# Kernel tuning notes

Hardware: AMD Instinct MI355X
Metric: run time of the kernel (lower is better)

The kernel has to match this reference:

```python
import jax, jax.numpy as jnp
import numpy as np

N_HEAD = 16


def setup_inputs() -> dict:
    key = jax.random.key(0)
    k1, k2, k3 = jax.random.split(key, 3)
    B, S, D = 4, 2048, 1024
    scale = 1.0 / np.sqrt(D)
    return {
        "inp": jax.random.normal(k1, (B, S, D), dtype=jnp.float32),
        "w_attn": jax.random.normal(k2, (D, 3 * D), dtype=jnp.float32) * scale,
        "b_attn": jnp.zeros((3 * D,), dtype=jnp.float32),
        "w_proj": jax.random.normal(k3, (D, D), dtype=jnp.float32) * scale,
        "b_proj": jnp.zeros((D,), dtype=jnp.float32),
    }


def reference(inp, w_attn, b_attn, w_proj, b_proj):
    B, S, D = inp.shape
    H = N_HEAD
    hd = D // H
    qkv = inp @ w_attn + b_attn                      # [B,S,3D]
    q, k, v = jnp.split(qkv, 3, axis=-1)
    q = q.reshape(B, S, H, hd)
    k = k.reshape(B, S, H, hd)
    v = v.reshape(B, S, H, hd)
    # scores [B,H,S,S], scaled by 1/sqrt(head_dim)
    scores = jnp.einsum("bqhd,bkhd->bhqk", q, k) / jnp.sqrt(jnp.asarray(hd, dtype=inp.dtype))
    # causal mask: position q attends to k <= q
    causal = jnp.tril(jnp.ones((S, S), dtype=bool))
    scores = jnp.where(causal[None, None], scores, jnp.asarray(-jnp.inf, dtype=scores.dtype))
    probs = jax.nn.softmax(scores, axis=-1)          # dropout omitted (eval mode)
    ctx = jnp.einsum("bhqk,bkhd->bqhd", probs, v).reshape(B, S, D)
    return ctx @ w_proj + b_proj
```

## Files before the change

kernel.cpp:

```cpp
#include <hip/hip_runtime.h>


#define DEV __device__ __forceinline__

typedef unsigned short u16;
typedef unsigned u32x4 __attribute__((ext_vector_type(4)));
typedef u16   u16x8 __attribute__((ext_vector_type(8)));
typedef u16   u16x4 __attribute__((ext_vector_type(4)));
typedef float f32x4v __attribute__((ext_vector_type(4)));
typedef __bf16 bf16x8 __attribute__((ext_vector_type(8)));

#define BB 4
#define SS 2048
#define DD 1024
#define HH 16
#define HD 64
#define MM (BB*SS)
#define N3D (3*DD)
#define C8  0.18033688011112042f

DEV u16 f2bf(float f) { return __builtin_bit_cast(u16, (__bf16)f); }
DEV float bf2f(u16 h) { return __builtin_bit_cast(float, (unsigned)h << 16); }

DEV f32x4v mfma16(u16x8 a, u16x8 b, f32x4v c) {
  return __builtin_amdgcn_mfma_f32_16x16x32_bf16(
      __builtin_bit_cast(bf16x8, a), __builtin_bit_cast(bf16x8, b), c, 0, 0, 0);
}

DEV void async16(const void* g, void* l) {
  __builtin_amdgcn_global_load_lds(
      (const __attribute__((address_space(1))) void*)g,
      (__attribute__((address_space(3))) void*)l, 16, 0, 0);
}

__global__ __launch_bounds__(256) void prep_kernel(
    const float* __restrict__ inp, const float* __restrict__ w_attn,
    const float* __restrict__ w_proj, u16* __restrict__ Abf,
    u16* __restrict__ WAt, u16* __restrict__ WPt) {
  const int bid = blockIdx.x;
  const int tid = threadIdx.x;
  if (bid < 4096) {
    __shared__ float t[32][33];
    const float* W; u16* Wt; int N, K, n0, k0;
    if (bid < 3072) { W = w_attn; Wt = WAt; N = N3D; K = DD;
                      n0 = (bid % 96) * 32; k0 = (bid / 96) * 32; }
    else            { W = w_proj; Wt = WPt; N = DD;  K = DD;
                      int tb = bid - 3072; n0 = (tb % 32) * 32; k0 = (tb / 32) * 32; }
    int tx = tid & 31, ty = tid >> 5;
    for (int i = ty; i < 32; i += 8)
      t[i][tx] = W[(long long)(k0 + i) * N + n0 + tx];
    __syncthreads();
    for (int i = ty; i < 32; i += 8)
      Wt[(long long)(n0 + i) * K + k0 + tx] = f2bf(t[tx][i]);
  } else {
    const long long n = (long long)MM * DD;
    long long i = (long long)(bid - 4096) * 256 + tid;
    for (long long j = i * 4; j < n; j += 2048LL * 256 * 4) {
      f32x4v v = *(const f32x4v*)(inp + j);
      u16x4 o;
      o.x = f2bf(v.x); o.y = f2bf(v.y); o.z = f2bf(v.z); o.w = f2bf(v.w);
      *(u16x4*)(Abf + j) = o;
    }
  }
}

__global__ __launch_bounds__(256) void gemm_kernel(
    const u16* __restrict__ A, const u16* __restrict__ Bt,
    const float* __restrict__ bias, void* __restrict__ Cout,
    u16* __restrict__ Vt, int Ndim, int Kdim, int mode) {
  __shared__ __align__(16) char smem[65536];

  const int tid = threadIdx.x;
  const int lane = tid & 63, wid = tid >> 6;
  const int l15 = lane & 15, lg = lane >> 4;

  const int nwg = (int)(gridDim.x * gridDim.y);
  const int orig = (int)(blockIdx.y * gridDim.x + blockIdx.x);
  const int wg = (orig & 7) * (nwg >> 3) + (orig >> 3);
  const int bx = wg % (int)gridDim.x, by = wg / (int)gridDim.x;
  const int rb = by * 128, cb = bx * 128;
  const int wr = (wid >> 1) * 64, wc = (wid & 1) * 64;

  f32x4v acc[4][4] = {};

  const int rlo = tid >> 3;
  const int cbS = (tid & 7) * 16;
  const int swS = cbS ^ ((rlo & 7) << 4);
  const int sd  = rlo * 128 + cbS;

  const int xr  = (l15 & 7) << 4;
  const int vaA = l15 * 128 + ((lg * 16) ^ xr);
  const int gvA0 = wr * 128 + vaA, gvA1 = gvA0 ^ 64;
  const int gvB0 = wc * 128 + vaA, gvB1 = gvB0 ^ 64;

  const char* pa[4];
  const char* pb[4];
#pragma unroll
  for (int i = 0; i < 4; ++i) {
    pa[i] = (const char*)A  + (long long)(rb + i * 32 + rlo) * (Kdim * 2) + swS;
    pb[i] = (const char*)Bt + (long long)(cb + i * 32 + rlo) * (Kdim * 2) + swS;
  }

  auto stage = [&](int dofs, int kb) {
#pragma unroll
    for (int i = 0; i < 4; ++i) {
      async16(pa[i] + kb, smem + dofs + i * 4096 + sd);
      async16(pb[i] + kb, smem + 32768 + dofs + i * 4096 + sd);
    }
  };

  auto compute = [&](int aofs, int bofs) {
    u16x8 a0[4], b0[4], a1[4], b1[4];
#pragma unroll
    for (int mi = 0; mi < 4; ++mi) {
      a0[mi] = *(const u16x8*)(smem + aofs + mi * 2048 + gvA0);
      a1[mi] = *(const u16x8*)(smem + aofs + mi * 2048 + gvA1);
    }
#pragma unroll
    for (int ni = 0; ni < 4; ++ni) {
      b0[ni] = *(const u16x8*)(smem + bofs + ni * 2048 + gvB0);
      b1[ni] = *(const u16x8*)(smem + bofs + ni * 2048 + gvB1);
    }
#pragma unroll
    for (int mi = 0; mi < 4; ++mi)
#pragma unroll
      for (int ni = 0; ni < 4; ++ni) {
        acc[mi][ni] = mfma16(a0[mi], b0[ni], acc[mi][ni]);
        acc[mi][ni] = mfma16(a1[mi], b1[ni], acc[mi][ni]);
      }
  };

  const int nK = Kdim >> 6;
  stage(0, 0);
  __syncthreads();
  for (int kt = 0; kt < nK; kt += 2) {
    stage(16384, 128);
    compute(0, 32768);
    __syncthreads();
    if (kt + 2 < nK) stage(0, 256);
    compute(16384, 49152);
    __syncthreads();
#pragma unroll
    for (int i = 0; i < 4; ++i) { pa[i] += 256; pb[i] += 256; }
  }

#pragma unroll
  for (int mi = 0; mi < 4; ++mi)
#pragma unroll
    for (int ni = 0; ni < 4; ++ni) {
      int col = cb + wc + ni * 16 + l15;
      float bv = bias[col];
      if (mode == 1 && col >= 2 * DD) {
        int h = (col >> 6) & 15, d = col & 63;
#pragma unroll
        for (int r = 0; r < 4; ++r) {
          int row = rb + wr + mi * 16 + lg * 4 + r;
          int b = row >> 11, s = row & 2047;
          Vt[(((long long)(b * HH + h) * HD + d) << 11) + s] = f2bf(acc[mi][ni][r] + bv);
        }
      } else {
#pragma unroll
        for (int r = 0; r < 4; ++r) {
          int row = rb + wr + mi * 16 + lg * 4 + r;
          float v = acc[mi][ni][r] + bv;
          if (mode) ((u16*)Cout)[(long long)row * Ndim + col] = f2bf(v);
          else      ((float*)Cout)[(long long)row * Ndim + col] = v;
        }
      }
    }
}

__global__ __launch_bounds__(256, 4) void attn_kernel(
    const u16* __restrict__ qkv, const u16* __restrict__ Vt,
    u16* __restrict__ ctx) {
  __shared__ __align__(16) char smem[32768];

  const int tid = threadIdx.x, lane = tid & 63, wid = tid >> 6;
  const int l15 = lane & 15, lg = lane >> 4;

  const int d = (int)blockIdx.x;
  const int rank = d >> 3;
  const int t = rank >> 3;
  const int jj = t & 3, q4 = t >> 2;
  const int qt = (q4 == 0) ? 15 - jj : (q4 == 1) ? 8 + jj
               : (q4 == 2) ? 7 - jj  : jj;
  const int bh = (d & 7) * 8 + (rank & 7);
  const int b = bh >> 4, h = bh & 15;

  const u16* Qcol = qkv + (long long)b * SS * N3D + h * HD;
  const u16* Kcol = qkv + (long long)b * SS * N3D + DD + h * HD;
  const u16* Vbh  = Vt + (long long)bh * HD * SS;

  const int rowA = 8 * (l15 >> 2) + (l15 & 3);
  const int kA = (((l15 & 3) | (((l15 >> 2) & 1) << 2))) << 4;
  const int vk0 = rowA * 128 + ((lg * 16) ^ kA);
  const int vk1 = vk0 ^ 64;
  const int vk2 = vk0 + 512;
  const int vk3 = vk2 ^ 64;
  const int kV = (((l15 & 3) | (((l15 >> 3) & 1) << 2))) << 4;
  const int vv0 = l15 * 128 + ((lg * 16) ^ kV);
  const int vv1 = vv0 ^ 64;

  const int rlo = tid >> 3;
  const int cbS = (tid & 7) * 16;
  const int kw = (((rlo & 3) | (((rlo >> 3) & 1) << 2))) << 4;
  const int swS = cbS ^ kw;
  const int sd  = rlo * 128 + cbS;
  const long long KSTP = 64LL * N3D * 2;
  const long long VSTP = 64LL * 2;
  const long long KHLF = 32LL * N3D * 2;
  const long long VHLF = 32LL * SS * 2;

  auto stage = [&](int dofs, const char* ka, const char* va) {
    async16(ka,        smem + dofs + sd);
    async16(ka + KHLF, smem + dofs + 4096 + sd);
    async16(va,        smem + 16384 + dofs + sd);
    async16(va + VHLF, smem + 16384 + dofs + 4096 + sd);
  };

  const int q0 = qt * 128;
  const int qw = q0 + wid * 32;
  const int nkb = 2 * qt + 2;

  u16x8 qf[2][2];
#pragma unroll
  for (int mi = 0; mi < 2; ++mi)
#pragma unroll
    for (int kk = 0; kk < 2; ++kk)
      qf[mi][kk] = *(const u16x8*)(Qcol + (long long)(qw + mi * 16 + l15) * N3D +
                                   kk * 32 + lg * 8);

  f32x4v acc[2][4] = {};
  float m_s[2] = {-1e30f, -1e30f}, l_p[2] = {0.f, 0.f};

  const char* ka = (const char*)Kcol + (long long)rlo * (N3D * 2) + swS;
  const char* va = (const char*)Vbh + (long long)rlo * (SS * 2) + swS;

  auto compute = [&](int kofs, int vofs, int kbase) {
    if (kbase > qw + 31) return;

    f32x4v pf[2][2][2] = {};
    {
      u16x8 kf0, kf1;
      kf0 = *(const u16x8*)(smem + kofs + vk0);
      kf1 = *(const u16x8*)(smem + kofs + vk1);
      __builtin_amdgcn_s_setprio(1);
      pf[0][0][0] = mfma16(kf0, qf[0][0], pf[0][0][0]);
      pf[0][0][0] = mfma16(kf1, qf[0][1], pf[0][0][0]);
      pf[1][0][0] = mfma16(kf0, qf[1][0], pf[1][0][0]);
      pf[1][0][0] = mfma16(kf1, qf[1][1], pf[1][0][0]);
      __builtin_amdgcn_s_setprio(0);
      kf0 = *(const u16x8*)(smem + kofs + vk2);
      kf1 = *(const u16x8*)(smem + kofs + vk3);
      __builtin_amdgcn_s_setprio(1);
      pf[0][0][1] = mfma16(kf0, qf[0][0], pf[0][0][1]);
      pf[0][0][1] = mfma16(kf1, qf[0][1], pf[0][0][1]);
      pf[1][0][1] = mfma16(kf0, qf[1][0], pf[1][0][1]);
      pf[1][0][1] = mfma16(kf1, qf[1][1], pf[1][0][1]);
      __builtin_amdgcn_s_setprio(0);
      kf0 = *(const u16x8*)(smem + kofs + 4096 + vk0);
      kf1 = *(const u16x8*)(smem + kofs + 4096 + vk1);
      __builtin_amdgcn_s_setprio(1);
      pf[0][1][0] = mfma16(kf0, qf[0][0], pf[0][1][0]);
      pf[0][1][0] = mfma16(kf1, qf[0][1], pf[0][1][0]);
      pf[1][1][0] = mfma16(kf0, qf[1][0], pf[1][1][0]);
      pf[1][1][0] = mfma16(kf1, qf[1][1], pf[1][1][0]);
      __builtin_amdgcn_s_setprio(0);
      kf0 = *(const u16x8*)(smem + kofs + 4096 + vk2);
      kf1 = *(const u16x8*)(smem + kofs + 4096 + vk3);
      __builtin_amdgcn_s_setprio(1);
      pf[0][1][1] = mfma16(kf0, qf[0][0], pf[0][1][1]);
      pf[0][1][1] = mfma16(kf1, qf[0][1], pf[0][1][1]);
      pf[1][1][1] = mfma16(kf0, qf[1][0], pf[1][1][1]);
      pf[1][1][1] = mfma16(kf1, qf[1][1], pf[1][1][1]);
      __builtin_amdgcn_s_setprio(0);
    }

    if (kbase + 63 > qw) {
      const int kl = kbase + lg * 8;
#pragma unroll
      for (int mi = 0; mi < 2; ++mi) {
        const int qg = qw + mi * 16 + l15;
#pragma unroll
        for (int ks = 0; ks < 2; ++ks)
#pragma unroll
          for (int ab = 0; ab < 2; ++ab)
#pragma unroll
            for (int r = 0; r < 4; ++r)
              if (kl + ks * 32 + ab * 4 + r > qg) pf[mi][ks][ab][r] = -1e30f;
      }
    }

    float lmax[2];
    bool need = false;
#pragma unroll
    for (int mi = 0; mi < 2; ++mi) {
      float v0 = fmaxf(fmaxf(fmaxf(pf[mi][0][0][0], pf[mi][0][0][1]),
                             pf[mi][0][0][2]), pf[mi][0][0][3]);
      float v1 = fmaxf(fmaxf(fmaxf(pf[mi][0][1][0], pf[mi][0][1][1]),
                             pf[mi][0][1][2]), pf[mi][0][1][3]);
      float v2 = fmaxf(fmaxf(fmaxf(pf[mi][1][0][0], pf[mi][1][0][1]),
                             pf[mi][1][0][2]), pf[mi][1][0][3]);
      float v3 = fmaxf(fmaxf(fmaxf(pf[mi][1][1][0], pf[mi][1][1][1]),
                             pf[mi][1][1][2]), pf[mi][1][1][3]);
      lmax[mi] = fmaxf(fmaxf(v0, v1), fmaxf(v2, v3));
      need = need || (lmax[mi] > m_s[mi] + 64.f);
    }
    if (__any(need)) {
#pragma unroll
      for (int mi = 0; mi < 2; ++mi) {
        float rm = fmaxf(lmax[mi], __shfl_xor(lmax[mi], 16));
        rm = fmaxf(rm, __shfl_xor(rm, 32));
        float newm = fmaxf(m_s[mi], rm);
        float sc = __builtin_exp2f((m_s[mi] - newm) * C8);
        m_s[mi] = newm;
        l_p[mi] *= sc;
#pragma unroll
        for (int r = 0; r < 4; ++r) {
          float scq = __shfl(sc, (lane & 48) + lg * 4 + r);
#pragma unroll
          for (int di = 0; di < 4; ++di) acc[mi][di][r] *= scq;
        }
      }
    }
#pragma unroll
    for (int mi = 0; mi < 2; ++mi) {
      float mC = m_s[mi] * C8;
      float rsum = 0.f;
#pragma unroll
      for (int ks = 0; ks < 2; ++ks)
#pragma unroll
        for (int ab = 0; ab < 2; ++ab)
#pragma unroll
          for (int r = 0; r < 4; ++r) {
            float p = __builtin_exp2f(__builtin_fmaf(pf[mi][ks][ab][r], C8, -mC));
            pf[mi][ks][ab][r] = p;
            rsum += p;
          }
      l_p[mi] += rsum;
    }

    u16x8 pa[2][2];
#pragma unroll
    for (int mi = 0; mi < 2; ++mi)
#pragma unroll
      for (int ks = 0; ks < 2; ++ks) {
        u32x4 w;
        w.x = (unsigned)f2bf(pf[mi][ks][0][0]) | ((unsigned)f2bf(pf[mi][ks][0][1]) << 16);
        w.y = (unsigned)f2bf(pf[mi][ks][0][2]) | ((unsigned)f2bf(pf[mi][ks][0][3]) << 16);
        w.z = (unsigned)f2bf(pf[mi][ks][1][0]) | ((unsigned)f2bf(pf[mi][ks][1][1]) << 16);
        w.w = (unsigned)f2bf(pf[mi][ks][1][2]) | ((unsigned)f2bf(pf[mi][ks][1][3]) << 16);
        pa[mi][ks] = __builtin_bit_cast(u16x8, w);
      }

#pragma unroll
    for (int di = 0; di < 4; ++di) {
      u16x8 v0 = *(const u16x8*)(smem + vofs + di * 2048 + vv0);
      u16x8 v1 = *(const u16x8*)(smem + vofs + di * 2048 + vv1);
      __builtin_amdgcn_s_setprio(1);
      acc[0][di] = mfma16(pa[0][0], v0, acc[0][di]);
      acc[0][di] = mfma16(pa[0][1], v1, acc[0][di]);
      acc[1][di] = mfma16(pa[1][0], v0, acc[1][di]);
      acc[1][di] = mfma16(pa[1][1], v1, acc[1][di]);
      __builtin_amdgcn_s_setprio(0);
    }
  };

  stage(0, ka, va);
  __syncthreads();

  for (int kb = 0; kb < nkb; kb += 2) {
    stage(8192, ka + KSTP, va + VSTP);
    compute(0, 16384, kb * 64);
    __syncthreads();
    if (kb + 2 < nkb) stage(0, ka + 2 * KSTP, va + 2 * VSTP);
    compute(8192, 24576, (kb + 1) * 64);
    __syncthreads();
    ka += 2 * KSTP; va += 2 * VSTP;
  }

#pragma unroll
  for (int mi = 0; mi < 2; ++mi) {
    float l_red = l_p[mi] + __shfl_xor(l_p[mi], 16);
    l_red += __shfl_xor(l_red, 32);
#pragma unroll
    for (int r = 0; r < 4; ++r) {
      float lq = __shfl(l_red, (lane & 48) + lg * 4 + r);
      float inv = 1.f / lq;
      int qrow = qw + mi * 16 + lg * 4 + r;
#pragma unroll
      for (int di = 0; di < 4; ++di) {
        int dd = di * 16 + l15;
        ctx[((long long)(b * SS + qrow)) * DD + h * HD + dd] = f2bf(acc[mi][di][r] * inv);
      }
    }
  }
}

extern "C" void kernel_launch(void* const* d_in, const int* in_sizes, int n_in,
                              void* d_out, int out_size, void* d_ws, size_t ws_size,
                              hipStream_t stream) {
  const float* inp    = (const float*)d_in[0];
  const float* w_attn = (const float*)d_in[1];
  const float* b_attn = (const float*)d_in[2];
  const float* w_proj = (const float*)d_in[3];
  const float* b_proj = (const float*)d_in[4];
  float* out = (float*)d_out;
  char* ws = (char*)d_ws;

  const long long off_A   = 0;
  const long long off_WAt = 16777216;
  const long long off_WPt = 23068672;
  const long long off_qkv = 25165824;
  const long long off_ctx = 75497472;
  const long long off_Vt  = 92274688;
  const long long need    = 109051904;
  if (ws_size < (size_t)need) return;

  u16* Abf = (u16*)(ws + off_A);
  u16* WAt = (u16*)(ws + off_WAt);
  u16* WPt = (u16*)(ws + off_WPt);
  u16* qkv = (u16*)(ws + off_qkv);
  u16* ctx = (u16*)(ws + off_ctx);
  u16* Vt  = (u16*)(ws + off_Vt);

  prep_kernel<<<6144, 256, 0, stream>>>(inp, w_attn, w_proj, Abf, WAt, WPt);
  gemm_kernel<<<dim3(N3D / 128, MM / 128), 256, 0, stream>>>(
      Abf, WAt, b_attn, qkv, Vt, N3D, DD, 1);
  attn_kernel<<<1024, 256, 0, stream>>>(qkv, Vt, ctx);
  gemm_kernel<<<dim3(DD / 128, MM / 128), 256, 0, stream>>>(
      ctx, WPt, b_proj, out, nullptr, DD, DD, 0);
}
```

Before: 175.5 us.

## Keep two async tile loads in flight with partial vmcnt waits in GEMM and attention

Both the GEMM and attention main loops now issue the next stage's async global-to-LDS loads before computing on the current buffer. They wait only on the older batch using s_waitcnt vmcnt(N) plus raw barriers instead of full __syncthreads, so loads overlap compute more deeply, and a peeled epilogue drains the pipeline. The attention block-to-q-tile mapping is also reshuffled to pair tiles differently for causal load balance. The hard-coded vmcnt values depend on the exact number of loads per stage, so a miscount would introduce a race.

```diff
diff --git a/kernel.cpp b/kernel.cpp
--- a/kernel.cpp
+++ b/kernel.cpp
@@ -32,6 +32,9 @@
       (const __attribute__((address_space(1))) void*)g,
       (__attribute__((address_space(3))) void*)l, 16, 0, 0);
 }
+
+#define WAIT_VM(N) asm volatile("s_waitcnt vmcnt(" #N ")" ::: "memory")
+#define BAR() __builtin_amdgcn_s_barrier()
 
 __global__ __launch_bounds__(256) void prep_kernel(
     const float* __restrict__ inp, const float* __restrict__ w_attn,
@@ -132,17 +135,24 @@
 
   const int nK = Kdim >> 6;
   stage(0, 0);
-  __syncthreads();
-  for (int kt = 0; kt < nK; kt += 2) {
-    stage(16384, 128);
+  stage(16384, 128);
+  int kt = 0;
+  for (; kt + 2 < nK; kt += 2) {
+    WAIT_VM(8); BAR();
     compute(0, 32768);
-    __syncthreads();
-    if (kt + 2 < nK) stage(0, 256);
+    BAR();
+    stage(0, 256);
+    WAIT_VM(8); BAR();
     compute(16384, 49152);
-    __syncthreads();
+    BAR();
+    stage(16384, 384);
 #pragma unroll
     for (int i = 0; i < 4; ++i) { pa[i] += 256; pb[i] += 256; }
   }
+  WAIT_VM(8); BAR();
+  compute(0, 32768);
+  WAIT_VM(0); BAR();
+  compute(16384, 49152);
 
 #pragma unroll
   for (int mi = 0; mi < 4; ++mi)
@@ -182,8 +192,8 @@
   const int rank = d >> 3;
   const int t = rank >> 3;
   const int jj = t & 3, q4 = t >> 2;
-  const int qt = (q4 == 0) ? 15 - jj : (q4 == 1) ? 8 + jj
-               : (q4 == 2) ? 7 - jj  : jj;
+  const int qt = (q4 == 0) ? 15 - 2 * jj : (q4 == 1) ? 14 - 2 * jj
+               : (q4 == 2) ? 1 + 2 * jj  : 2 * jj;
   const int bh = (d & 7) * 8 + (rank & 7);
   const int b = bh >> 4, h = bh & 15;
 
@@ -367,17 +377,24 @@
   };
 
   stage(0, ka, va);
-  __syncthreads();
-
-  for (int kb = 0; kb < nkb; kb += 2) {
-    stage(8192, ka + KSTP, va + VSTP);
+  stage(8192, ka + KSTP, va + VSTP);
+
+  int kb = 0;
+  for (; kb + 2 < nkb; kb += 2) {
+    WAIT_VM(4); BAR();
     compute(0, 16384, kb * 64);
-    __syncthreads();
-    if (kb + 2 < nkb) stage(0, ka + 2 * KSTP, va + 2 * VSTP);
+    BAR();
+    stage(0, ka + 2 * KSTP, va + 2 * VSTP);
+    WAIT_VM(4); BAR();
     compute(8192, 24576, (kb + 1) * 64);
-    __syncthreads();
+    BAR();
+    stage(8192, ka + 3 * KSTP, va + 3 * VSTP);
     ka += 2 * KSTP; va += 2 * VSTP;
   }
+  WAIT_VM(4); BAR();
+  compute(0, 16384, kb * 64);
+  WAIT_VM(0); BAR();
+  compute(8192, 24576, (kb + 1) * 64);
 
 #pragma unroll
   for (int mi = 0; mi < 2; ++mi) {
```

New measurement: 172.6 us. No clear change (-1.6%).
